# Kernel optimization log

Measured on AMD Instinct MI355X. Metric: run time of the kernel, lower is better.

## Reference

```python
import jax, jax.numpy as jnp
import numpy as np

# Faithful reference for NaiveKmeans._cost / one assignment step of forward:
# squared Euclidean distances (torch.cdist(x, centers)**2) followed by a
# row-wise min (costs) and argmin (cluster indices).
# Note: the original module's host-side while-loop re-seeds centers as
# x[indices] (shape (N,d)), which is a bug that explodes to an NxN cdist;
# the kernel-relevant, well-defined math is this single cdist^2 + min step,
# which we implement here (it is exactly what forward computes before the loop).

def setup_inputs() -> dict:
    key = jax.random.key(0)
    kx, kc = jax.random.split(key)
    x = jax.random.normal(kx, (131072, 128), dtype=jnp.float32)
    centers = jax.random.normal(kc, (1024, 128), dtype=jnp.float32)
    return {"x": x, "centers": centers}


def _sq_cdist(x, c):
    x2 = jnp.sum(x * x, axis=1, keepdims=True)        # [N, 1]
    c2 = jnp.sum(c * c, axis=1)                       # [K]
    d2 = x2 + c2 - 2.0 * (x @ c.T)                    # [N, K]
    return jnp.maximum(d2, 0.0)


def reference(x, centers):
    d2 = _sq_cdist(x, centers)          # [N, K] squared distances
    costs = jnp.min(d2, axis=1)         # [N] per-point cost
    indices = jnp.argmin(d2, axis=1)    # [N] cluster assignment
    return costs, indices
```

## Files before the change

### kernel.cpp

```cpp
#include <hip/hip_runtime.h>


typedef _Float16 f16x8 __attribute__((ext_vector_type(8)));
typedef float    f32x4 __attribute__((ext_vector_type(4)));
typedef unsigned short u16;

constexpr int N = 131072, D = 128, K = 1024;
constexpr int MT = 128;

union H2U { _Float16 h; unsigned short u; };

__device__ inline void gl_lds16(const void* g, void* l) {
  __builtin_amdgcn_global_load_lds(
      (const __attribute__((address_space(1))) unsigned int*)g,
      (__attribute__((address_space(3))) unsigned int*)l, 16, 0, 0);
}

__global__ void prep_centers(const float* __restrict__ centers,
                             u16* __restrict__ Bh, u16* __restrict__ Bl,
                             float* __restrict__ c2) {
  const int wave = threadIdx.x >> 6, lane = threadIdx.x & 63;
  const int c = blockIdx.x * 4 + wave;
  const float2 v = ((const float2*)(centers + (size_t)c * D))[lane];
  float s = v.x * v.x + v.y * v.y;
  #pragma unroll
  for (int off = 32; off; off >>= 1) s += __shfl_xor(s, off, 64);
  if (lane == 0) c2[c] = s;

  H2U h0, h1, l0, l1;
  h0.h = (_Float16)v.x;  l0.h = (_Float16)(v.x - (float)h0.h);
  h1.h = (_Float16)v.y;  l1.h = (_Float16)(v.y - (float)h1.h);
  const int cb = c >> 7, cm = c & 127;
  const int kc = lane >> 4, q = (lane >> 2) & 3, j0 = (lane & 3) * 2;
  const size_t off = (((size_t)(cb * 4 + kc) * 4 + q) * 128 + cm) * 8 + j0;
  *(unsigned*)(Bh + off) = (unsigned)h0.u | ((unsigned)h1.u << 16);
  *(unsigned*)(Bl + off) = (unsigned)l0.u | ((unsigned)l1.u << 16);
}

__global__ __launch_bounds__(256, 2) void kmeans_mfma(
    const float* __restrict__ x,
    const u16* __restrict__ Bh_g, const u16* __restrict__ Bl_g,
    const float* __restrict__ c2g,
    float* __restrict__ out_cost, float* __restrict__ out_idx)
{
  __shared__ __align__(16) u16 smem[40960];
  u16* Ah = smem;
  u16* Al = smem + 16384;

  const int tid = threadIdx.x;
  const int wave = tid >> 6, lane = tid & 63;
  const int wr = wave >> 1, wc = wave & 1;
  const int q = lane >> 4, ln = lane & 15;
  const int m0 = blockIdx.x * MT;

  #pragma unroll
  for (int i = 0; i < 16; ++i) {
    const int flat = i * 256 + tid;
    const int m = flat >> 5, c4 = flat & 31, k0 = c4 * 4;
    const float4 v = *(const float4*)(x + (size_t)(m0 + m) * D + k0);
    const int kc = k0 >> 5, qq = (k0 >> 3) & 3, j0 = k0 & 7;
    const float vv[4] = {v.x, v.y, v.z, v.w};
    H2U h[4], l[4];
    #pragma unroll
    for (int z = 0; z < 4; ++z) {
      h[z].h = (_Float16)vv[z];
      l[z].h = (_Float16)(vv[z] - (float)h[z].h);
    }
    const int off = ((kc * 4 + qq) * 128 + m) * 8 + j0;
    uint2 hp, lp;
    hp.x = h[0].u | ((unsigned)h[1].u << 16); hp.y = h[2].u | ((unsigned)h[3].u << 16);
    lp.x = l[0].u | ((unsigned)l[1].u << 16); lp.y = l[2].u | ((unsigned)l[3].u << 16);
    *(uint2*)(Ah + off) = hp;
    *(uint2*)(Al + off) = lp;
  }
  __syncthreads();

  float x2m = 0.f;
  if (tid < MT) {
    #pragma unroll
    for (int kq = 0; kq < 16; ++kq) {
      const f16x8 hv = *(const f16x8*)(Ah + (kq * 128 + tid) * 8);
      const f16x8 lv = *(const f16x8*)(Al + (kq * 128 + tid) * 8);
      #pragma unroll
      for (int e = 0; e < 8; ++e) {
        const float xv = (float)hv[e] + (float)lv[e];
        x2m += xv * xv;
      }
    }
  }

  auto stageBh = [&](int cc, int p) {
    const size_t gbase = (size_t)cc * 4096;
    u16* buf = smem + 32768 + p * 4096;
    #pragma unroll
    for (int i = 0; i < 2; ++i) {
      const size_t eoff = (size_t)i * 2048 + (size_t)wave * 512;
      gl_lds16(Bh_g + gbase + eoff + (size_t)lane * 8, buf + eoff);
    }
  };
  auto blPtr = [&](int cc, int t) {
    return (const f16x8*)(Bl_g +
        ((size_t)(cc * 4 + q) * 128 + wc * 64 + t * 16 + ln) * 8);
  };

  float bestV[16]; int bestI[16];
  #pragma unroll
  for (int b = 0; b < 16; ++b) { bestV[b] = 3.4e38f; bestI[b] = 0; }

  stageBh(0, 0);
  f16x8 blc[4], bln[4];
  #pragma unroll
  for (int t = 0; t < 4; ++t) blc[t] = *blPtr(0, t);

  for (int ct = 0; ct < 8; ++ct) {
    f32x4 acc[4][4];
    #pragma unroll
    for (int mt = 0; mt < 4; ++mt)
      #pragma unroll
      for (int nt = 0; nt < 4; ++nt)
        acc[mt][nt] = (f32x4){0.f, 0.f, 0.f, 0.f};

    float c2v[4];
    #pragma unroll
    for (int nt = 0; nt < 4; ++nt)
      c2v[nt] = c2g[ct * 128 + wc * 64 + nt * 16 + ln];

    #pragma unroll
    for (int kc = 0; kc < 4; ++kc) {
      const int cc = ct * 4 + kc;
      __syncthreads();
      if (cc < 31) {
        stageBh(cc + 1, (cc + 1) & 1);
        #pragma unroll
        for (int t = 0; t < 4; ++t) bln[t] = *blPtr(cc + 1, t);
      }
      const u16* buf = smem + 32768 + (cc & 1) * 4096;

      f16x8 ah[4], al[4], bh[4];
      #pragma unroll
      for (int t = 0; t < 4; ++t) {
        const int moff = ((kc * 4 + q) * 128 + wr * 64 + t * 16 + ln) * 8;
        ah[t] = *(const f16x8*)(Ah + moff);
        al[t] = *(const f16x8*)(Al + moff);
        bh[t] = *(const f16x8*)(buf + (q * 128 + wc * 64 + t * 16 + ln) * 8);
      }
      #pragma unroll
      for (int mt = 0; mt < 4; ++mt)
        #pragma unroll
        for (int nt = 0; nt < 4; ++nt)
          acc[mt][nt] = __builtin_amdgcn_mfma_f32_16x16x32_f16(ah[mt], bh[nt], acc[mt][nt], 0, 0, 0);
      #pragma unroll
      for (int mt = 0; mt < 4; ++mt)
        #pragma unroll
        for (int nt = 0; nt < 4; ++nt)
          acc[mt][nt] = __builtin_amdgcn_mfma_f32_16x16x32_f16(al[mt], bh[nt], acc[mt][nt], 0, 0, 0);
      #pragma unroll
      for (int mt = 0; mt < 4; ++mt)
        #pragma unroll
        for (int nt = 0; nt < 4; ++nt)
          acc[mt][nt] = __builtin_amdgcn_mfma_f32_16x16x32_f16(ah[mt], blc[nt], acc[mt][nt], 0, 0, 0);
      #pragma unroll
      for (int t = 0; t < 4; ++t) blc[t] = bln[t];
    }

    #pragma unroll
    for (int nt = 0; nt < 4; ++nt) {
      const int n = ct * 128 + wc * 64 + nt * 16 + ln;
      #pragma unroll
      for (int mt = 0; mt < 4; ++mt)
        #pragma unroll
        for (int r = 0; r < 4; ++r) {
          const float s = __builtin_fmaf(-2.f, acc[mt][nt][r], c2v[nt]);
          const int b = mt * 4 + r;
          if (s < bestV[b]) { bestV[b] = s; bestI[b] = n; }
        }
    }
  }

  #pragma unroll
  for (int b = 0; b < 16; ++b) {
    float v = bestV[b]; int idx = bestI[b];
    #pragma unroll
    for (int off = 1; off < 16; off <<= 1) {
      const float ov = __shfl_xor(v, off, 64);
      const int   oi = __shfl_xor(idx, off, 64);
      if (ov < v || (ov == v && oi < idx)) { v = ov; idx = oi; }
    }
    bestV[b] = v; bestI[b] = idx;
  }

  __syncthreads();
  float* redV = (float*)(smem + 32768);
  int*   redI = (int*)(smem + 33280);
  if (ln == 0) {
    #pragma unroll
    for (int b = 0; b < 16; ++b) {
      const int ml = wr * 64 + (b >> 2) * 16 + q * 4 + (b & 3);
      redV[ml * 2 + wc] = bestV[b];
      redI[ml * 2 + wc] = bestI[b];
    }
  }
  __syncthreads();
  if (tid < MT) {
    float v = redV[tid * 2]; int idx = redI[tid * 2];
    const float v1 = redV[tid * 2 + 1]; const int i1 = redI[tid * 2 + 1];
    if (v1 < v || (v1 == v && i1 < idx)) { v = v1; idx = i1; }
    float cost = x2m + v;
    if (cost < 0.f) cost = 0.f;
    out_cost[m0 + tid] = cost;
    out_idx[m0 + tid]  = (float)idx;
  }
}

extern "C" void kernel_launch(void* const* d_in, const int* in_sizes, int n_in,
                              void* d_out, int out_size, void* d_ws, size_t ws_size,
                              hipStream_t stream) {
  const float* x       = (const float*)d_in[0];
  const float* centers = (const float*)d_in[1];
  u16*   Bh = (u16*)d_ws;
  u16*   Bl = Bh + (size_t)K * D;
  float* c2 = (float*)(Bl + (size_t)K * D);
  float* out_cost = (float*)d_out;
  float* out_idx  = out_cost + N;

  prep_centers<<<K / 4, 256, 0, stream>>>(centers, Bh, Bl, c2);
  kmeans_mfma<<<N / MT, 256, 0, stream>>>(x, Bh, Bl, c2, out_cost, out_idx);
}
```

Before: 180.7 us.

## Load center tiles directly into registers, drop per-step barriers, swizzle A in LDS

Replaces the LDS double-buffered staging of the high-half center tiles with per-wave register prefetch from global memory, like the low half already uses, which removes the block-wide barrier on every k-chunk. Adds an XOR swizzle to the A tile LDS layout to reduce bank conflicts and raises wave priority around the MFMA bursts. The trade-off is duplicated global/L2 reads of the center data across waves sharing a column and more registers held for prefetch.

```diff
diff --git a/kernel.cpp b/kernel.cpp
--- a/kernel.cpp
+++ b/kernel.cpp
@@ -9,12 +9,6 @@
 constexpr int MT = 128;
 
 union H2U { _Float16 h; unsigned short u; };
-
-__device__ inline void gl_lds16(const void* g, void* l) {
-  __builtin_amdgcn_global_load_lds(
-      (const __attribute__((address_space(1))) unsigned int*)g,
-      (__attribute__((address_space(3))) unsigned int*)l, 16, 0, 0);
-}
 
 __global__ void prep_centers(const float* __restrict__ centers,
                              u16* __restrict__ Bh, u16* __restrict__ Bl,
@@ -43,7 +37,7 @@
     const float* __restrict__ c2g,
     float* __restrict__ out_cost, float* __restrict__ out_idx)
 {
-  __shared__ __align__(16) u16 smem[40960];
+  __shared__ __align__(16) u16 smem[33792];
   u16* Ah = smem;
   u16* Al = smem + 16384;
 
@@ -58,7 +52,8 @@
     const int flat = i * 256 + tid;
     const int m = flat >> 5, c4 = flat & 31, k0 = c4 * 4;
     const float4 v = *(const float4*)(x + (size_t)(m0 + m) * D + k0);
-    const int kc = k0 >> 5, qq = (k0 >> 3) & 3, j0 = k0 & 7;
+    const int g = k0 >> 3;
+    const int j0 = k0 & 7;
     const float vv[4] = {v.x, v.y, v.z, v.w};
     H2U h[4], l[4];
     #pragma unroll
@@ -66,7 +61,7 @@
       h[z].h = (_Float16)vv[z];
       l[z].h = (_Float16)(vv[z] - (float)h[z].h);
     }
-    const int off = ((kc * 4 + qq) * 128 + m) * 8 + j0;
+    const int off = ((g * 128 + m) * 8 + j0) ^ ((g & 7) << 3);
     uint2 hp, lp;
     hp.x = h[0].u | ((unsigned)h[1].u << 16); hp.y = h[2].u | ((unsigned)h[3].u << 16);
     lp.x = l[0].u | ((unsigned)l[1].u << 16); lp.y = l[2].u | ((unsigned)l[3].u << 16);
@@ -78,9 +73,10 @@
   float x2m = 0.f;
   if (tid < MT) {
     #pragma unroll
-    for (int kq = 0; kq < 16; ++kq) {
-      const f16x8 hv = *(const f16x8*)(Ah + (kq * 128 + tid) * 8);
-      const f16x8 lv = *(const f16x8*)(Al + (kq * 128 + tid) * 8);
+    for (int g = 0; g < 16; ++g) {
+      const int off = ((g * 128 + tid) * 8) ^ ((g & 7) << 3);
+      const f16x8 hv = *(const f16x8*)(Ah + off);
+      const f16x8 lv = *(const f16x8*)(Al + off);
       #pragma unroll
       for (int e = 0; e < 8; ++e) {
         const float xv = (float)hv[e] + (float)lv[e];
@@ -89,14 +85,9 @@
     }
   }
 
-  auto stageBh = [&](int cc, int p) {
-    const size_t gbase = (size_t)cc * 4096;
-    u16* buf = smem + 32768 + p * 4096;
-    #pragma unroll
-    for (int i = 0; i < 2; ++i) {
-      const size_t eoff = (size_t)i * 2048 + (size_t)wave * 512;
-      gl_lds16(Bh_g + gbase + eoff + (size_t)lane * 8, buf + eoff);
-    }
+  auto bhPtr = [&](int cc, int t) {
+    return (const f16x8*)(Bh_g +
+        ((size_t)(cc * 4 + q) * 128 + wc * 64 + t * 16 + ln) * 8);
   };
   auto blPtr = [&](int cc, int t) {
     return (const f16x8*)(Bl_g +
@@ -107,10 +98,9 @@
   #pragma unroll
   for (int b = 0; b < 16; ++b) { bestV[b] = 3.4e38f; bestI[b] = 0; }
 
-  stageBh(0, 0);
-  f16x8 blc[4], bln[4];
-  #pragma unroll
-  for (int t = 0; t < 4; ++t) blc[t] = *blPtr(0, t);
+  f16x8 bhc[4], blc[4], bhn[4], bln[4];
+  #pragma unroll
+  for (int t = 0; t < 4; ++t) { bhc[t] = *bhPtr(0, t); blc[t] = *blPtr(0, t); }
 
   for (int ct = 0; ct < 8; ++ct) {
     f32x4 acc[4][4];
@@ -128,39 +118,43 @@
     #pragma unroll
     for (int kc = 0; kc < 4; ++kc) {
       const int cc = ct * 4 + kc;
-      __syncthreads();
       if (cc < 31) {
-        stageBh(cc + 1, (cc + 1) & 1);
-        #pragma unroll
-        for (int t = 0; t < 4; ++t) bln[t] = *blPtr(cc + 1, t);
+        #pragma unroll
+        for (int t = 0; t < 4; ++t) {
+          bhn[t] = *bhPtr(cc + 1, t);
+          bln[t] = *blPtr(cc + 1, t);
+        }
       }
-      const u16* buf = smem + 32768 + (cc & 1) * 4096;
-
-      f16x8 ah[4], al[4], bh[4];
+
+      f16x8 ah[4], al[4];
       #pragma unroll
       for (int t = 0; t < 4; ++t) {
-        const int moff = ((kc * 4 + q) * 128 + wr * 64 + t * 16 + ln) * 8;
+        const int gg = kc * 4 + q;
+        const int moff = ((gg * 128 + wr * 64 + t * 16 + ln) * 8) ^ ((gg & 7) << 3);
         ah[t] = *(const f16x8*)(Ah + moff);
         al[t] = *(const f16x8*)(Al + moff);
-        bh[t] = *(const f16x8*)(buf + (q * 128 + wc * 64 + t * 16 + ln) * 8);
       }
+
+      __builtin_amdgcn_s_setprio(1);
       #pragma unroll
       for (int mt = 0; mt < 4; ++mt)
         #pragma unroll
         for (int nt = 0; nt < 4; ++nt)
-          acc[mt][nt] = __builtin_amdgcn_mfma_f32_16x16x32_f16(ah[mt], bh[nt], acc[mt][nt], 0, 0, 0);
+          acc[mt][nt] = __builtin_amdgcn_mfma_f32_16x16x32_f16(ah[mt], bhc[nt], acc[mt][nt], 0, 0, 0);
       #pragma unroll
       for (int mt = 0; mt < 4; ++mt)
         #pragma unroll
         for (int nt = 0; nt < 4; ++nt)
-          acc[mt][nt] = __builtin_amdgcn_mfma_f32_16x16x32_f16(al[mt], bh[nt], acc[mt][nt], 0, 0, 0);
+          acc[mt][nt] = __builtin_amdgcn_mfma_f32_16x16x32_f16(al[mt], bhc[nt], acc[mt][nt], 0, 0, 0);
       #pragma unroll
       for (int mt = 0; mt < 4; ++mt)
         #pragma unroll
         for (int nt = 0; nt < 4; ++nt)
           acc[mt][nt] = __builtin_amdgcn_mfma_f32_16x16x32_f16(ah[mt], blc[nt], acc[mt][nt], 0, 0, 0);
-      #pragma unroll
-      for (int t = 0; t < 4; ++t) blc[t] = bln[t];
+      __builtin_amdgcn_s_setprio(0);
+
+      #pragma unroll
+      for (int t = 0; t < 4; ++t) { bhc[t] = bhn[t]; blc[t] = bln[t]; }
     }
 
     #pragma unroll
@@ -189,7 +183,6 @@
     bestV[b] = v; bestI[b] = idx;
   }
 
-  __syncthreads();
   float* redV = (float*)(smem + 32768);
   int*   redI = (int*)(smem + 33280);
   if (ln == 0) {
```

Result: slower. 375.1 us (+107.5%).
